# Kernel optimization log

Hardware: AMD Instinct MI355X
Metric: run time of the kernel (lower is better)

Reference implementation:

```python
import jax, jax.numpy as jnp
import numpy as np

B, L, D = 16, 2048, 512
MAXC = L // 2 + 1  # static upper bound on #segments: strict local minima can't be adjacent, +1 for forced start at t=0


def _uma_pool(xs_pad, w_lin, b_lin):
    # xs_pad: [B, L, D]
    Ll = xs_pad.shape[1]
    w = jax.nn.sigmoid(jnp.einsum('bld,d->bl', xs_pad, w_lin) + b_lin[0])  # [B, L] uma weights
    before = jnp.pad(w[:, :-1], ((0, 0), (1, 0)))  # zero-pad left, like torch F.pad
    after = jnp.pad(w[:, 1:], ((0, 0), (0, 1)))    # zero-pad right
    minima = (w < before) & (w < after)  # always False at t=0 and t=L-1 since sigmoid(w) > 0
    start_mask = minima.at[:, 0].set(True)   # mask[:,0] = True for starts
    end_mask = minima.at[:, -1].set(True)    # mask[:,-1] = True for ends (mask[:,0] already False)
    t = jnp.arange(Ll)
    # gather per-batch valley positions into padded [B, MAXC] arrays (sentinel = L, sorted to front-pack)
    start_pos = jnp.sort(jnp.where(start_mask, t, Ll), axis=1)[:, :MAXC]
    end_pos = jnp.sort(jnp.where(end_mask, t, Ll), axis=1)[:, :MAXC]
    valid = start_pos < Ll
    starts = jnp.where(valid, start_pos, 0)
    ends = jnp.where(valid, jnp.minimum(end_pos + 2, Ll), 0)  # segment is [start, end); padded rows -> empty
    # output_mask[b,m,t] = 1 if starts[b,m] <= t < ends[b,m]  (== utri[end] - utri[start] in torch)
    seg = ((t[None, None, :] >= starts[:, :, None]) & (t[None, None, :] < ends[:, :, None])).astype(xs_pad.dtype)
    seg = jax.lax.stop_gradient(seg)  # torch detaches output_mask
    numer = jnp.einsum('bml,bld->bmd', seg, xs_pad * w[..., None])   # bmm(mask, alpha_h)
    denom = jnp.maximum(jnp.einsum('bml,bl->bm', seg, w)[..., None], 1e-6)  # bmm(mask, w).clamp_(1e-6)
    return numer / denom  # [B, MAXC, D]; rows beyond actual valley count are exactly 0


def setup_inputs() -> dict:
    key = jax.random.key(0)
    k1, k2, k3 = jax.random.split(key, 3)
    xs_pad = jax.random.normal(k1, (B, L, D), dtype=jnp.float32)
    w_lin = jax.random.normal(k2, (D,), dtype=jnp.float32) * 0.05  # Linear(D,1).weight
    b_lin = jax.random.normal(k3, (1,), dtype=jnp.float32) * 0.05  # Linear(D,1).bias
    olens = jnp.full((B,), L, dtype=jnp.int32)  # full-length utterances; olens[0] is the longest
    return {"xs_pad": xs_pad, "w_lin": w_lin, "b_lin": b_lin, "olens": olens}


def reference(xs_pad, w_lin, b_lin, olens):
    out = _uma_pool(xs_pad, w_lin, b_lin)
    olens_out = (olens.astype(jnp.float32) / olens[0].astype(jnp.float32) * out.shape[1]).astype(olens.dtype)
    return (out, olens_out)
```

## Files before the change

### kernel.cpp

```cpp
#include <hip/hip_runtime.h>

#define B 16
#define L 2048
#define D 512
#define MAXC 1025

__global__ __launch_bounds__(256) void k_weights(const float* __restrict__ xs,
                                                 const float* __restrict__ w_lin,
                                                 const float* __restrict__ b_lin,
                                                 float* __restrict__ w_out) {
    const int wave = threadIdx.x >> 6;
    const int lane = threadIdx.x & 63;
    const int row = blockIdx.x * 4 + wave;
    if (row >= B * L) return;

    const float4* x4  = (const float4*)(xs + (size_t)row * D);
    const float4* wl4 = (const float4*)w_lin;

    float4 a0 = x4[lane];
    float4 c0 = wl4[lane];
    float p = a0.x * c0.x + a0.y * c0.y + a0.z * c0.z + a0.w * c0.w;
    float4 a1 = x4[lane + 64];
    float4 c1 = wl4[lane + 64];
    p += a1.x * c1.x + a1.y * c1.y + a1.z * c1.z + a1.w * c1.w;

    #pragma unroll
    for (int off = 32; off > 0; off >>= 1) p += __shfl_xor(p, off, 64);

    if (lane == 0) {
        float z = p + b_lin[0];
        w_out[row] = 1.0f / (1.0f + expf(-z));
    }
}

__global__ __launch_bounds__(256) void k_segments(const float* __restrict__ w,
                                                  int* __restrict__ starts,
                                                  int* __restrict__ ends,
                                                  int* __restrict__ count,
                                                  const int* __restrict__ olens,
                                                  float* __restrict__ olens_out) {
    const int b = blockIdx.x;
    const int tid = threadIdx.x;
    const float* wb = w + (size_t)b * L;

    int pos[4];
    int lcnt = 0;
    const int t0 = tid * 8;
    #pragma unroll
    for (int i = 0; i < 8; ++i) {
        int t = t0 + i;
        if (t >= 1 && t <= L - 2) {
            float c = wb[t];
            if (c < wb[t - 1] && c < wb[t + 1]) pos[lcnt++] = t;
        }
    }

    __shared__ int scn[256];
    scn[tid] = lcnt;
    __syncthreads();
    #pragma unroll
    for (int s = 1; s < 256; s <<= 1) {
        int v = (tid >= s) ? scn[tid - s] : 0;
        __syncthreads();
        scn[tid] += v;
        __syncthreads();
    }
    const int excl = scn[tid] - lcnt;
    const int total = scn[255];

    for (int i = 0; i < lcnt; ++i) {
        int j = excl + i;
        int t = pos[i];
        starts[b * MAXC + j + 1] = t;
        int e = t + 2;
        ends[b * MAXC + j] = (e < L) ? e : L;
    }
    if (tid == 0) {
        starts[b * MAXC + 0] = 0;
        ends[b * MAXC + total] = L;
        count[b] = total + 1;
        int v = (int)((float)olens[b] / (float)olens[0] * (float)MAXC);
        olens_out[b] = (float)v;
    }
}

__global__ __launch_bounds__(128) void k_pool(const float* __restrict__ xs,
                                              const float* __restrict__ w,
                                              const int* __restrict__ starts,
                                              const int* __restrict__ ends,
                                              const int* __restrict__ count,
                                              float* __restrict__ out) {
    const int m = blockIdx.x;
    const int b = blockIdx.y;
    const int tid = threadIdx.x;

    float4* out4 = (float4*)(out + (size_t)(b * MAXC + m) * D);

    if (m >= count[b]) {
        out4[tid] = make_float4(0.f, 0.f, 0.f, 0.f);
        return;
    }

    const int s = starts[b * MAXC + m];
    const int e = ends[b * MAXC + m];
    const float* wb = w + (size_t)b * L;
    const float4* x4 = (const float4*)(xs + (size_t)b * L * D);

    float4 acc = make_float4(0.f, 0.f, 0.f, 0.f);
    float dsum = 0.f;
    for (int t = s; t < e; ++t) {
        float wt = wb[t];
        dsum += wt;
        float4 x = x4[(size_t)t * (D / 4) + tid];
        acc.x += x.x * wt;
        acc.y += x.y * wt;
        acc.z += x.z * wt;
        acc.w += x.w * wt;
    }
    float inv = 1.0f / fmaxf(dsum, 1e-6f);
    out4[tid] = make_float4(acc.x * inv, acc.y * inv, acc.z * inv, acc.w * inv);
}

extern "C" void kernel_launch(void* const* d_in, const int* in_sizes, int n_in,
                              void* d_out, int out_size, void* d_ws, size_t ws_size,
                              hipStream_t stream) {
    const float* xs    = (const float*)d_in[0];
    const float* w_lin = (const float*)d_in[1];
    const float* b_lin = (const float*)d_in[2];
    const int*   olens = (const int*)d_in[3];

    float* out = (float*)d_out;
    float* olens_out = (float*)d_out + (size_t)B * MAXC * D;

    char* ws = (char*)d_ws;
    float* w_buf = (float*)ws;
    int* starts  = (int*)(ws + (size_t)B * L * sizeof(float));
    int* ends    = starts + B * MAXC;
    int* count   = ends + B * MAXC;

    k_weights<<<dim3((B * L) / 4), 256, 0, stream>>>(xs, w_lin, b_lin, w_buf);
    k_segments<<<dim3(B), 256, 0, stream>>>(w_buf, starts, ends, count, olens, olens_out);
    k_pool<<<dim3(MAXC, B), 128, 0, stream>>>(xs, w_buf, starts, ends, count, out);
}
```

Before: 122.0 us.

## Fuse weight, segment and pool stages into one cooperative persistent kernel

Replaces the three kernel launches with a single cooperative kernel of 1024 blocks that computes the sigmoid weights with a grid-stride loop, uses grid-wide syncs between stages, runs the segment scan on the first 16 blocks, and pools segments over a persistent loop. The aim is to remove the launch overheads and inter-kernel gaps. In exchange, two grid-wide barriers are added and most blocks sit idle during the segment stage. The old three-kernel path is kept as a fallback if the cooperative launch fails.

```diff
diff --git a/kernel.cpp b/kernel.cpp
--- a/kernel.cpp
+++ b/kernel.cpp
@@ -1,9 +1,130 @@
 #include <hip/hip_runtime.h>
+#include <hip/hip_cooperative_groups.h>
+
+namespace cg = cooperative_groups;
 
 #define B 16
 #define L 2048
 #define D 512
 #define MAXC 1025
+#define NBLK 1024
+#define NTHR 256
+
+__global__ __launch_bounds__(NTHR, 4) void k_fused(
+    const float* __restrict__ xs, const float* __restrict__ w_lin,
+    const float* __restrict__ b_lin, const int* __restrict__ olens,
+    float* __restrict__ out, float* __restrict__ olens_out,
+    float* __restrict__ w_buf, int* __restrict__ starts,
+    int* __restrict__ ends, int* __restrict__ count)
+{
+    cg::grid_group grid = cg::this_grid();
+    const int tid = threadIdx.x;
+    const int wave = tid >> 6;
+    const int lane = tid & 63;
+
+    {
+        const float4* wl4 = (const float4*)w_lin;
+        const float4 c0 = wl4[lane];
+        const float4 c1 = wl4[lane + 64];
+        const float bias = b_lin[0];
+        const int gw = blockIdx.x * 4 + wave;
+        #pragma unroll
+        for (int it = 0; it < 8; ++it) {
+            const int row = gw + 4096 * it;
+            const float4* x4 = (const float4*)(xs + (size_t)row * D);
+            float4 a0 = x4[lane];
+            float4 a1 = x4[lane + 64];
+            float p = a0.x * c0.x + a0.y * c0.y + a0.z * c0.z + a0.w * c0.w
+                    + a1.x * c1.x + a1.y * c1.y + a1.z * c1.z + a1.w * c1.w;
+            #pragma unroll
+            for (int off = 32; off > 0; off >>= 1) p += __shfl_xor(p, off, 64);
+            if (lane == 0) w_buf[row] = 1.0f / (1.0f + expf(-(p + bias)));
+        }
+    }
+
+    grid.sync();
+
+    __shared__ int scn[NTHR];
+    if (blockIdx.x < B) {
+        const int b = blockIdx.x;
+        const float* wb = w_buf + (size_t)b * L;
+
+        int pos[4];
+        int lcnt = 0;
+        const int t0 = tid * 8;
+        #pragma unroll
+        for (int i = 0; i < 8; ++i) {
+            int t = t0 + i;
+            if (t >= 1 && t <= L - 2) {
+                float c = wb[t];
+                if (c < wb[t - 1] && c < wb[t + 1]) pos[lcnt++] = t;
+            }
+        }
+
+        scn[tid] = lcnt;
+        __syncthreads();
+        #pragma unroll
+        for (int s = 1; s < NTHR; s <<= 1) {
+            int v = (tid >= s) ? scn[tid - s] : 0;
+            __syncthreads();
+            scn[tid] += v;
+            __syncthreads();
+        }
+        const int excl = scn[tid] - lcnt;
+        const int total = scn[NTHR - 1];
+
+        for (int i = 0; i < lcnt; ++i) {
+            int j = excl + i;
+            int t = pos[i];
+            starts[b * MAXC + j + 1] = t;
+            int e = t + 2;
+            ends[b * MAXC + j] = (e < L) ? e : L;
+        }
+        if (tid == 0) {
+            starts[b * MAXC + 0] = 0;
+            ends[b * MAXC + total] = L;
+            count[b] = total + 1;
+            int v = (int)((float)olens[b] / (float)olens[0] * (float)MAXC);
+            olens_out[b] = (float)v;
+        }
+    }
+
+    grid.sync();
+
+    {
+        const int sub = tid >> 7;
+        const int st  = tid & 127;
+        for (int r = blockIdx.x * 2 + sub; r < B * MAXC; r += NBLK * 2) {
+            const int b = r / MAXC;
+            const int m = r - b * MAXC;
+            float4* out4 = (float4*)(out + (size_t)r * D);
+
+            if (m >= count[b]) {
+                out4[st] = make_float4(0.f, 0.f, 0.f, 0.f);
+                continue;
+            }
+
+            const int s = starts[b * MAXC + m];
+            const int e = ends[b * MAXC + m];
+            const float* wb = w_buf + (size_t)b * L;
+            const float4* x4 = (const float4*)(xs + (size_t)b * L * D);
+
+            float4 acc = make_float4(0.f, 0.f, 0.f, 0.f);
+            float dsum = 0.f;
+            for (int t = s; t < e; ++t) {
+                float wt = wb[t];
+                dsum += wt;
+                float4 x = x4[(size_t)t * (D / 4) + st];
+                acc.x += x.x * wt;
+                acc.y += x.y * wt;
+                acc.z += x.z * wt;
+                acc.w += x.w * wt;
+            }
+            float inv = 1.0f / fmaxf(dsum, 1e-6f);
+            out4[st] = make_float4(acc.x * inv, acc.y * inv, acc.z * inv, acc.w * inv);
+        }
+    }
+}
 
 __global__ __launch_bounds__(256) void k_weights(const float* __restrict__ xs,
                                                  const float* __restrict__ w_lin,
@@ -138,7 +259,16 @@
     int* ends    = starts + B * MAXC;
     int* count   = ends + B * MAXC;
 
-    k_weights<<<dim3((B * L) / 4), 256, 0, stream>>>(xs, w_lin, b_lin, w_buf);
-    k_segments<<<dim3(B), 256, 0, stream>>>(w_buf, starts, ends, count, olens, olens_out);
-    k_pool<<<dim3(MAXC, B), 128, 0, stream>>>(xs, w_buf, starts, ends, count, out);
-}
+    void* args[] = {
+        (void*)&xs, (void*)&w_lin, (void*)&b_lin, (void*)&olens,
+        (void*)&out, (void*)&olens_out, (void*)&w_buf,
+        (void*)&starts, (void*)&ends, (void*)&count
+    };
+    hipError_t err = hipLaunchCooperativeKernel((const void*)k_fused, dim3(NBLK),
+                                                dim3(NTHR), args, 0, stream);
+    if (err != hipSuccess) {
+        k_weights<<<dim3((B * L) / 4), 256, 0, stream>>>(xs, w_lin, b_lin, w_buf);
+        k_segments<<<dim3(B), 256, 0, stream>>>(w_buf, starts, ends, count, olens, olens_out);
+        k_pool<<<dim3(MAXC, B), 128, 0, stream>>>(xs, w_buf, starts, ends, count, out);
+    }
+}
```

Result: slower. 318.6 us (+161.2%).
